# Kernel tuning notes

Measured on AMD Instinct MI355X. Metric: run time of the kernel, lower is better.

The kernel has to match this reference:

```python
import jax, jax.numpy as jnp
import numpy as np

B, S_T, P, D = 2, 8, 1369, 1024
S_STUDENT = 4
R = 128    # num_ref_samples
NS = 128   # num_shared_samples
K = 4      # topk
STUDENT_FRAMES = (0, 2, 4, 6)
EXTRA_FRAMES = (1, 3, 5, 7)   # teacher-only frames
HUBER_DELTA = 1.0
W1 = W2 = W3 = 1.0


def setup_inputs() -> dict:
    key = jax.random.key(0)
    k1, k2, k3, k4 = jax.random.split(key, 4)
    teacher_feats = jax.random.normal(k1, (B, S_T, P, D), dtype=jnp.float32)
    student_feats = jax.random.normal(k2, (B, S_STUDENT, P, D), dtype=jnp.float32)
    ref_perm = jax.random.permutation(k3, P)[:R].astype(jnp.int32)
    shared_perm = jax.random.permutation(k4, P)[:NS].astype(jnp.int32)
    return {"teacher_feats": teacher_feats, "student_feats": student_feats,
            "ref_perm": ref_perm, "shared_perm": shared_perm}


def _unit(x, eps):
    # F.normalize(x, dim=-1, eps=eps)
    n = jnp.linalg.norm(x, axis=-1, keepdims=True)
    return x / jnp.maximum(n, eps)


def _huber(pred, target):
    d = pred - target
    ad = jnp.abs(d)
    return jnp.where(ad < HUBER_DELTA, 0.5 * d * d, HUBER_DELTA * (ad - 0.5 * HUBER_DELTA))


def reference(teacher_feats, student_feats, ref_perm, shared_perm):
    t = jax.lax.stop_gradient(teacher_feats)  # teacher is always detached
    eps = 1e-8

    ref_t = t[:, STUDENT_FRAMES[0], ref_perm, :]        # [B,R,D]
    ref_s = student_feats[:, 0, ref_perm, :]            # [B,R,D]

    # top-K most similar teacher patches across extra frames
    extra_t = t[:, jnp.array(EXTRA_FRAMES)].reshape(B, len(EXTRA_FRAMES) * P, D)  # [B,M,D]
    sim = jnp.einsum('brd,bmd->brm', _unit(ref_t, 1e-12), _unit(extra_t, 1e-12))
    _, idx = jax.lax.top_k(sim, K)                      # [B,R,K]
    sim_high = jnp.take_along_axis(
        extra_t, idx.reshape(B, R * K)[:, :, None], axis=1).reshape(B, R, K, D)

    # vertex-ref / vertex-simhigh legs that don't depend on the shared frame
    b1_t = _unit(sim_high - ref_t[:, :, None, :], eps)  # [B,R,K,D]
    b1_s = _unit(sim_high - ref_s[:, :, None, :], eps)
    u2_t = _unit(ref_t[:, :, None, :] - sim_high, eps)  # [B,R,K,D]
    u2_s = _unit(ref_s[:, :, None, :] - sim_high, eps)

    s1 = jnp.float32(0.0)
    s2 = jnp.float32(0.0)
    s3 = jnp.float32(0.0)
    for f, t_idx in enumerate(STUDENT_FRAMES[1:]):
        sh_t = t[:, t_idx, shared_perm, :]              # [B,S,D]
        sh_s = student_feats[:, f + 1, shared_perm, :]  # [B,S,D]

        # angle1: vertex = ref; cos(shared-ref, simhigh-ref)
        a1_t = jnp.einsum('brsd,brkd->brsk', _unit(sh_t[:, None] - ref_t[:, :, None], eps), b1_t)
        a1_s = jnp.einsum('brsd,brkd->brsk', _unit(sh_s[:, None] - ref_s[:, :, None], eps), b1_s)
        s1 = s1 + _huber(a1_s, jax.lax.stop_gradient(a1_t)).sum()

        # angle2: vertex = sim_high; cos(ref-simhigh, shared-simhigh)
        v2_t = _unit(sh_t[:, None, :, None, :] - sim_high[:, :, None], eps)  # [B,R,S,K,D]
        v2_s = _unit(sh_s[:, None, :, None, :] - sim_high[:, :, None], eps)
        a2_t = jnp.einsum('brkd,brskd->brsk', u2_t, v2_t)
        a2_s = jnp.einsum('brkd,brskd->brsk', u2_s, v2_s)
        s2 = s2 + _huber(a2_s, jax.lax.stop_gradient(a2_t)).sum()

        # angle3: vertex = shared; cos(ref-shared, simhigh-shared)
        u3_t = _unit(ref_t[:, :, None] - sh_t[:, None], eps)                 # [B,R,S,D]
        u3_s = _unit(ref_s[:, :, None] - sh_s[:, None], eps)
        v3_t = _unit(sim_high[:, :, None] - sh_t[:, None, :, None, :], eps)  # [B,R,S,K,D]
        v3_s = _unit(sim_high[:, :, None] - sh_s[:, None, :, None, :], eps)
        a3_t = jnp.einsum('brsd,brskd->brsk', u3_t, v3_t)
        a3_s = jnp.einsum('brsd,brskd->brsk', u3_s, v3_s)
        s3 = s3 + _huber(a3_s, jax.lax.stop_gradient(a3_t)).sum()

    total = B * R * NS * K * len(STUDENT_FRAMES[1:])
    return W1 * s1 / total + W2 * s2 / total + W3 * s3 / total
```

## Files before the change

### kernel.cpp

```cpp
#include <hip/hip_runtime.h>
#include <float.h>

#define B_  2
#define ST_ 8
#define SS_ 4
#define P_  1369
#define D_  1024
#define R_  128
#define NS_ 128
#define K_  4
#define M_  5476

#define OFF_INVN  0u
#define OFF_REFT  11008u
#define OFF_REFS  (OFF_REFT + 262144u)
#define OFF_PRRT  (OFF_REFS + 262144u)
#define OFF_PRRS  (OFF_PRRT + 256u)
#define OFF_IDX   (OFF_PRRS + 256u)
#define OFF_PRST  (OFF_IDX + 1024u)
#define OFF_PRSS  (OFF_PRST + 1024u)
#define OFF_PSS   (OFF_PRSS + 1024u)
#define OFF_IB1T  (OFF_PSS + 1024u)
#define OFF_IB1S  (OFF_IB1T + 1024u)
#define OFF_NSH   (OFF_IB1S + 1024u)
#define OFF_C     (OFF_NSH + 1536u)
#define CP_       1401856u

__device__ __forceinline__ float dot4(const float4 a, const float4 b) {
  return a.x*b.x + a.y*b.y + a.z*b.z + a.w*b.w;
}

__global__ __launch_bounds__(256) void k_extra_norms(const float* __restrict__ teacher,
                                                     float* __restrict__ invn) {
  int row = blockIdx.x * 4 + (threadIdx.x >> 6);
  int lane = threadIdx.x & 63;
  if (row >= B_ * M_) return;
  int b = row / M_, m = row % M_;
  int j = m / P_, p = m % P_;
  const float* src = teacher + (((size_t)b * ST_ + 1 + 2 * j) * P_ + p) * D_;
  float s = 0.f;
  #pragma unroll
  for (int it = 0; it < 4; ++it) {
    float4 v = *(const float4*)(src + (it * 64 + lane) * 4);
    s += dot4(v, v);
  }
  for (int o = 32; o; o >>= 1) s += __shfl_down(s, o);
  if (lane == 0) invn[row] = 1.f / fmaxf(sqrtf(s), 1e-12f);
}

__global__ __launch_bounds__(256) void k_shnorm(const float* __restrict__ teacher,
                                                const float* __restrict__ student,
                                                const int* __restrict__ shared_perm,
                                                float* __restrict__ nsh) {
  int row = blockIdx.x * 4 + (threadIdx.x >> 6);
  int lane = threadIdx.x & 63;
  if (row >= 2 * B_ * 3 * NS_) return;
  int rid = row % (B_ * 3 * NS_);
  int is_stu = row / (B_ * 3 * NS_);
  int b = rid / (3 * NS_);
  int rem = rid % (3 * NS_);
  int f = rem / NS_, s = rem % NS_;
  int p = shared_perm[s];
  const float* src = is_stu
      ? student + (((size_t)b * SS_ + 1 + f) * P_ + p) * D_
      : teacher + (((size_t)b * ST_ + 2 + 2 * f) * P_ + p) * D_;
  float acc = 0.f;
  #pragma unroll
  for (int it = 0; it < 4; ++it) {
    float4 v = *(const float4*)(src + (it * 64 + lane) * 4);
    acc += dot4(v, v);
  }
  for (int o = 32; o; o >>= 1) acc += __shfl_down(acc, o);
  if (lane == 0) nsh[row] = acc;
}

__global__ __launch_bounds__(256) void k_ref_gather(const float* __restrict__ teacher,
                                                    const float* __restrict__ student,
                                                    const int* __restrict__ ref_perm,
                                                    float* __restrict__ reft,
                                                    float* __restrict__ refs,
                                                    float* __restrict__ prrt,
                                                    float* __restrict__ prrs) {
  int br = blockIdx.x;
  int b = br / R_, r = br % R_;
  int p = ref_perm[r];
  const float* st = teacher + (((size_t)b * ST_ + 0) * P_ + p) * D_;
  const float* ss = student + (((size_t)b * SS_ + 0) * P_ + p) * D_;
  float* dt = reft + (size_t)br * D_;
  float* dsp = refs + (size_t)br * D_;
  int t = threadIdx.x;
  float4 vt = *(const float4*)(st + t * 4);
  float4 vs = *(const float4*)(ss + t * 4);
  *(float4*)(dt + t * 4) = vt;
  *(float4*)(dsp + t * 4) = vs;
  float at = dot4(vt, vt);
  float as = dot4(vs, vs);
  for (int o = 32; o; o >>= 1) { at += __shfl_down(at, o); as += __shfl_down(as, o); }
  __shared__ float red[16];
  int w = t >> 6, lane = t & 63;
  if (lane == 0) { red[w] = at; red[8 + w] = as; }
  __syncthreads();
  if (t == 0) {
    prrt[br] = red[0] + red[1] + red[2] + red[3];
    prrs[br] = red[8] + red[9] + red[10] + red[11];
  }
}

__global__ __launch_bounds__(256) void k_sim_gemm(const float* __restrict__ teacher,
                                                  const float* __restrict__ reft,
                                                  float* __restrict__ Cp) {
  const int bid = blockIdx.x;
  const int kq  = bid & 3;
  const int rest = bid >> 2;
  const int b   = rest / 172;
  const int rem = rest % 172;
  const int rt  = rem / 86;
  const int mt  = rem % 86;
  const int r0 = rt * 64, m0 = mt * 64;
  __shared__ __align__(16) float Al[32 * 68];
  __shared__ __align__(16) float El[32 * 68];
  const int t = threadIdx.x;
  const int tx = t & 15, ty = t >> 4;
  const int lr = t >> 3;
  const int lk = (t & 7) * 4;
  const float* arow0 = reft + (size_t)(b * R_ + r0 + lr) * D_;
  const float* arow1 = reft + (size_t)(b * R_ + r0 + 32 + lr) * D_;
  const float* erow0; const float* erow1; bool ev0, ev1;
  {
    int m = m0 + lr; ev0 = m < M_;
    int mm = ev0 ? m : 0; int j = mm / P_, p = mm % P_;
    erow0 = teacher + (((size_t)b * ST_ + 1 + 2 * j) * P_ + p) * D_;
    m = m0 + 32 + lr; ev1 = m < M_;
    mm = ev1 ? m : 0; j = mm / P_; p = mm % P_;
    erow1 = teacher + (((size_t)b * ST_ + 1 + 2 * j) * P_ + p) * D_;
  }
  float acc[4][4];
  #pragma unroll
  for (int i = 0; i < 4; ++i)
    #pragma unroll
    for (int j = 0; j < 4; ++j) acc[i][j] = 0.f;

  const int kbeg = kq * 256, kend = kbeg + 256;
  for (int kc = kbeg; kc < kend; kc += 32) {
    __syncthreads();
    float4 a0 = *(const float4*)(arow0 + kc + lk);
    float4 a1 = *(const float4*)(arow1 + kc + lk);
    float4 e0 = ev0 ? *(const float4*)(erow0 + kc + lk) : make_float4(0, 0, 0, 0);
    float4 e1 = ev1 ? *(const float4*)(erow1 + kc + lk) : make_float4(0, 0, 0, 0);
    Al[(lk + 0) * 68 + lr] = a0.x; Al[(lk + 1) * 68 + lr] = a0.y;
    Al[(lk + 2) * 68 + lr] = a0.z; Al[(lk + 3) * 68 + lr] = a0.w;
    Al[(lk + 0) * 68 + 32 + lr] = a1.x; Al[(lk + 1) * 68 + 32 + lr] = a1.y;
    Al[(lk + 2) * 68 + 32 + lr] = a1.z; Al[(lk + 3) * 68 + 32 + lr] = a1.w;
    El[(lk + 0) * 68 + lr] = e0.x; El[(lk + 1) * 68 + lr] = e0.y;
    El[(lk + 2) * 68 + lr] = e0.z; El[(lk + 3) * 68 + lr] = e0.w;
    El[(lk + 0) * 68 + 32 + lr] = e1.x; El[(lk + 1) * 68 + 32 + lr] = e1.y;
    El[(lk + 2) * 68 + 32 + lr] = e1.z; El[(lk + 3) * 68 + 32 + lr] = e1.w;
    __syncthreads();
    #pragma unroll
    for (int kk = 0; kk < 32; ++kk) {
      float4 av = *(const float4*)&Al[kk * 68 + ty * 4];
      float4 ev = *(const float4*)&El[kk * 68 + tx * 4];
      acc[0][0] += av.x * ev.x; acc[0][1] += av.x * ev.y; acc[0][2] += av.x * ev.z; acc[0][3] += av.x * ev.w;
      acc[1][0] += av.y * ev.x; acc[1][1] += av.y * ev.y; acc[1][2] += av.y * ev.z; acc[1][3] += av.y * ev.w;
      acc[2][0] += av.z * ev.x; acc[2][1] += av.z * ev.y; acc[2][2] += av.z * ev.z; acc[2][3] += av.z * ev.w;
      acc[3][0] += av.w * ev.x; acc[3][1] += av.w * ev.y; acc[3][2] += av.w * ev.z; acc[3][3] += av.w * ev.w;
    }
  }
  const int mbase = m0 + tx * 4;
  float* cbase = Cp + (size_t)kq * CP_;
  #pragma unroll
  for (int i = 0; i < 4; ++i) {
    int r = r0 + ty * 4 + i;
    float* crow = cbase + (size_t)(b * R_ + r) * M_;
    if (mbase + 3 < M_) {
      *(float4*)(crow + mbase) = make_float4(acc[i][0], acc[i][1], acc[i][2], acc[i][3]);
    } else {
      if (mbase + 0 < M_) crow[mbase + 0] = acc[i][0];
      if (mbase + 1 < M_) crow[mbase + 1] = acc[i][1];
      if (mbase + 2 < M_) crow[mbase + 2] = acc[i][2];
      if (mbase + 3 < M_) crow[mbase + 3] = acc[i][3];
    }
  }
}

__device__ __forceinline__ void topk_insert(float v, int m, float bv[4], int bi[4]) {
  bool better3 = (v > bv[3]) || (v == bv[3] && m < bi[3]);
  if (!better3) return;
  int pos = 3;
  while (pos > 0) {
    bool better = (v > bv[pos - 1]) || (v == bv[pos - 1] && m < bi[pos - 1]);
    if (better) { bv[pos] = bv[pos - 1]; bi[pos] = bi[pos - 1]; --pos; }
    else break;
  }
  bv[pos] = v; bi[pos] = m;
}

__global__ __launch_bounds__(256) void k_topk(const float* __restrict__ Cp,
                                              const float* __restrict__ invn,
                                              int* __restrict__ idxout) {
  int br = blockIdx.x;
  int b = br / R_;
  const float* r0 = Cp + 0 * (size_t)CP_ + (size_t)br * M_;
  const float* r1 = Cp + 1 * (size_t)CP_ + (size_t)br * M_;
  const float* r2 = Cp + 2 * (size_t)CP_ + (size_t)br * M_;
  const float* r3 = Cp + 3 * (size_t)CP_ + (size_t)br * M_;
  const float* w = invn + (size_t)b * M_;
  int t = threadIdx.x;
  float bv[4] = {-FLT_MAX, -FLT_MAX, -FLT_MAX, -FLT_MAX};
  int   bi[4] = {0x7fffffff, 0x7fffffff, 0x7fffffff, 0x7fffffff};
  for (int m = t; m < M_; m += 256) {
    float v = ((r0[m] + r1[m]) + (r2[m] + r3[m])) * w[m];
    topk_insert(v, m, bv, bi);
  }

  #pragma unroll
  for (int o = 1; o < 64; o <<= 1) {
    float ov[4]; int oi[4];
    #pragma unroll
    for (int q = 0; q < 4; ++q) {
      ov[q] = __shfl_xor(bv[q], o);
      oi[q] = __shfl_xor(bi[q], o);
    }
    #pragma unroll
    for (int q = 0; q < 4; ++q) topk_insert(ov[q], oi[q], bv, bi);
  }

  __shared__ float sv[16];
  __shared__ int   si[16];
  int wv = t >> 6, lane = t & 63;
  if (lane == 0) {
    #pragma unroll
    for (int q = 0; q < 4; ++q) { sv[wv * 4 + q] = bv[q]; si[wv * 4 + q] = bi[q]; }
  }
  __syncthreads();
  if (t == 0) {
    float tv[4] = {-FLT_MAX, -FLT_MAX, -FLT_MAX, -FLT_MAX};
    int   ti[4] = {0x7fffffff, 0x7fffffff, 0x7fffffff, 0x7fffffff};
    #pragma unroll
    for (int e = 0; e < 16; ++e) topk_insert(sv[e], si[e], tv, ti);
    #pragma unroll
    for (int q = 0; q < 4; ++q) idxout[br * 4 + q] = ti[q];
  }
}

__global__ __launch_bounds__(256) void k_prep(const float* __restrict__ teacher,
                                              const float* __restrict__ reft,
                                              const float* __restrict__ refs,
                                              const int* __restrict__ idx,
                                              float* __restrict__ prst,
                                              float* __restrict__ prss,
                                              float* __restrict__ pss,
                                              float* __restrict__ ib1t,
                                              float* __restrict__ ib1s) {
  int br = blockIdx.x;
  int b = br / R_;
  int w = threadIdx.x >> 6, lane = threadIdx.x & 63;
  int m = idx[br * 4 + w];
  int j = m / P_, p = m % P_;
  const float* sim = teacher + (((size_t)b * ST_ + 1 + 2 * j) * P_ + p) * D_;
  const float* rt = reft + (size_t)br * D_;
  const float* rs = refs + (size_t)br * D_;
  float s_ss = 0, s_rt = 0, s_rs = 0, s_dt = 0, s_ds = 0;
  #pragma unroll
  for (int it = 0; it < 4; ++it) {
    int d = (it * 64 + lane) * 4;
    float4 svv = *(const float4*)(sim + d);
    float4 tvv = *(const float4*)(rt + d);
    float4 uvv = *(const float4*)(rs + d);
    s_ss += dot4(svv, svv);
    s_rt += dot4(svv, tvv);
    s_rs += dot4(svv, uvv);
    float4 dt = make_float4(svv.x - tvv.x, svv.y - tvv.y, svv.z - tvv.z, svv.w - tvv.w);
    float4 ds = make_float4(svv.x - uvv.x, svv.y - uvv.y, svv.z - uvv.z, svv.w - uvv.w);
    s_dt += dot4(dt, dt);
    s_ds += dot4(ds, ds);
  }
  for (int o = 32; o; o >>= 1) {
    s_ss += __shfl_down(s_ss, o); s_rt += __shfl_down(s_rt, o); s_rs += __shfl_down(s_rs, o);
    s_dt += __shfl_down(s_dt, o); s_ds += __shfl_down(s_ds, o);
  }
  if (lane == 0) {
    int o = br * 4 + w;
    pss[o] = s_ss; prst[o] = s_rt; prss[o] = s_rs;
    ib1t[o] = 1.f / fmaxf(sqrtf(s_dt), 1e-8f);
    ib1s[o] = 1.f / fmaxf(sqrtf(s_ds), 1e-8f);
  }
}

__device__ __forceinline__ float huber1(float d) {
  float ad = fabsf(d);
  return (ad < 1.0f) ? 0.5f * d * d : (ad - 0.5f);
}

__global__ __launch_bounds__(256) void k_loss(const float* __restrict__ teacher,
                                              const float* __restrict__ student,
                                              const int* __restrict__ shared_perm,
                                              const int* __restrict__ idx,
                                              const float* __restrict__ reft,
                                              const float* __restrict__ refs,
                                              const float* __restrict__ prrt,
                                              const float* __restrict__ prrs,
                                              const float* __restrict__ prst,
                                              const float* __restrict__ prss,
                                              const float* __restrict__ pss,
                                              const float* __restrict__ ib1t,
                                              const float* __restrict__ ib1s,
                                              const float* __restrict__ nsh,
                                              float* __restrict__ out) {
  int br = blockIdx.x, f = blockIdx.y, sc = blockIdx.z;
  int b = br / R_;
  int tf = 2 + 2 * f;
  int sf = 1 + f;
  __shared__ __align__(16) float Lsim[4][1024];
  __shared__ __align__(16) float Lrt[1024];
  __shared__ __align__(16) float Lrs[1024];
  __shared__ int sperm[128];
  __shared__ float Lns[2][64];
  __shared__ float scal[22];
  __shared__ float wred[4];
  int t = threadIdx.x;
  {
    const float* rt = reft + (size_t)br * D_;
    const float* rs = refs + (size_t)br * D_;
    *(float4*)&Lrt[t * 4] = *(const float4*)(rt + t * 4);
    *(float4*)&Lrs[t * 4] = *(const float4*)(rs + t * 4);
    #pragma unroll
    for (int k = 0; k < 4; ++k) {
      int m = idx[br * 4 + k]; int j = m / P_, p = m % P_;
      const float* sim = teacher + (((size_t)b * ST_ + 1 + 2 * j) * P_ + p) * D_;
      *(float4*)&Lsim[k][t * 4] = *(const float4*)(sim + t * 4);
    }
  }
  if (t < 128) sperm[t] = shared_perm[t];
  if (t < 64) {
    int o = (b * 3 + f) * NS_ + sc * 64 + t;
    Lns[0][t] = nsh[o];
    Lns[1][t] = nsh[B_ * 3 * NS_ + o];
  }
  if (t < 4) {
    int o = br * 4 + t;
    scal[t] = prst[o]; scal[4 + t] = prss[o]; scal[8 + t] = pss[o];
    scal[12 + t] = ib1t[o]; scal[16 + t] = ib1s[o];
  }
  if (t == 4) scal[20] = prrt[br];
  if (t == 5) scal[21] = prrs[br];
  __syncthreads();

  const int g = t >> 2, gl = t & 3;
  const int s = sc * 64 + g;
  const int p = sperm[s];
  const float* sht = teacher + (((size_t)b * ST_ + tf) * P_ + p) * D_;
  const float* shs = student + (((size_t)b * SS_ + sf) * P_ + p) * D_;

  float qt0 = 0, qt1 = 0, qt2 = 0, qt3 = 0, qtr = 0;
  float qs0 = 0, qs1 = 0, qs2 = 0, qs3 = 0, qsr = 0;
  #pragma unroll 2
  for (int i = 0; i < 64; ++i) {
    int off = i * 16 + gl * 4;
    float4 a  = *(const float4*)(sht + off);
    float4 c  = *(const float4*)(shs + off);
    float4 v0 = *(const float4*)&Lsim[0][off];
    float4 v1 = *(const float4*)&Lsim[1][off];
    float4 v2 = *(const float4*)&Lsim[2][off];
    float4 v3 = *(const float4*)&Lsim[3][off];
    float4 r1 = *(const float4*)&Lrt[off];
    float4 r2 = *(const float4*)&Lrs[off];
    qt0 += dot4(a, v0); qt1 += dot4(a, v1); qt2 += dot4(a, v2); qt3 += dot4(a, v3);
    qtr += dot4(a, r1);
    qs0 += dot4(c, v0); qs1 += dot4(c, v1); qs2 += dot4(c, v2); qs3 += dot4(c, v3);
    qsr += dot4(c, r2);
  }
  #pragma unroll
  for (int o = 1; o <= 2; o <<= 1) {
    qt0 += __shfl_xor(qt0, o); qt1 += __shfl_xor(qt1, o);
    qt2 += __shfl_xor(qt2, o); qt3 += __shfl_xor(qt3, o);
    qtr += __shfl_xor(qtr, o);
    qs0 += __shfl_xor(qs0, o); qs1 += __shfl_xor(qs1, o);
    qs2 += __shfl_xor(qs2, o); qs3 += __shfl_xor(qs3, o);
    qsr += __shfl_xor(qsr, o);
  }
  const int k = gl;
  float qsim  = (gl == 0) ? qt0 : (gl == 1) ? qt1 : (gl == 2) ? qt2 : qt3;
  float qsimS = (gl == 0) ? qs0 : (gl == 1) ? qs1 : (gl == 2) ? qs2 : qs3;
  float qref = qtr, qrefS = qsr;
  float qss = Lns[0][g], qssS = Lns[1][g];

  float Prs_t = scal[k], Prs_s = scal[4 + k], Pss_k = scal[8 + k];
  float ibt = scal[12 + k], ibs = scal[16 + k];
  float Prr_t = scal[20], Prr_s = scal[21];
  float n1sq = qss - 2.f * qref + Prr_t;
  float i1 = 1.f / fmaxf(sqrtf(fmaxf(n1sq, 0.f)), 1e-8f);
  float n2sq = qss - 2.f * qsim + Pss_k;
  float i2 = 1.f / fmaxf(sqrtf(fmaxf(n2sq, 0.f)), 1e-8f);
  float a1t = (qsim - qref - Prs_t + Prr_t) * ibt * i1;
  float a2t = -(qsim - Pss_k - qref + Prs_t) * ibt * i2;
  float a3t = (qss - qsim - qref + Prs_t) * i1 * i2;
  float n1sqS = qssS - 2.f * qrefS + Prr_s;
  float i1s = 1.f / fmaxf(sqrtf(fmaxf(n1sqS, 0.f)), 1e-8f);
  float n2sqS = qssS - 2.f * qsimS + Pss_k;
  float i2s = 1.f / fmaxf(sqrtf(fmaxf(n2sqS, 0.f)), 1e-8f);
  float a1s = (qsimS - qrefS - Prs_s + Prr_s) * ibs * i1s;
  float a2s = -(qsimS - Pss_k - qrefS + Prs_s) * ibs * i2s;
  float a3s = (qssS - qsimS - qrefS + Prs_s) * i1s * i2s;
  float lacc = huber1(a1s - a1t) + huber1(a2s - a2t) + huber1(a3s - a3t);

  int w = t >> 6, lane = t & 63;
  for (int o = 32; o; o >>= 1) lacc += __shfl_down(lacc, o);
  if (lane == 0) wred[w] = lacc;
  __syncthreads();
  if (t == 0) {
    float ssum = wred[0] + wred[1] + wred[2] + wred[3];
    atomicAdd(out, ssum * (1.0f / 393216.0f));
  }
}

extern "C" void kernel_launch(void* const* d_in, const int* in_sizes, int n_in,
                              void* d_out, int out_size, void* d_ws, size_t ws_size,
                              hipStream_t stream) {
  const float* teacher = (const float*)d_in[0];
  const float* student = (const float*)d_in[1];
  const int* ref_perm = (const int*)d_in[2];
  const int* shared_perm = (const int*)d_in[3];
  float* ws = (float*)d_ws;
  float* invn = ws + OFF_INVN;
  float* reft = ws + OFF_REFT;
  float* refs = ws + OFF_REFS;
  float* prrt = ws + OFF_PRRT;
  float* prrs = ws + OFF_PRRS;
  int*   idx  = (int*)(ws + OFF_IDX);
  float* prst = ws + OFF_PRST;
  float* prss = ws + OFF_PRSS;
  float* pss  = ws + OFF_PSS;
  float* ib1t = ws + OFF_IB1T;
  float* ib1s = ws + OFF_IB1S;
  float* nsh  = ws + OFF_NSH;
  float* Cp   = ws + OFF_C;

  hipMemsetAsync(d_out, 0, sizeof(float), stream);

  k_extra_norms<<<(B_ * M_ + 3) / 4, 256, 0, stream>>>(teacher, invn);
  k_shnorm<<<(2 * B_ * 3 * NS_ + 3) / 4, 256, 0, stream>>>(teacher, student,
                                                           shared_perm, nsh);
  k_ref_gather<<<B_ * R_, 256, 0, stream>>>(teacher, student, ref_perm,
                                            reft, refs, prrt, prrs);
  k_sim_gemm<<<1376, 256, 0, stream>>>(teacher, reft, Cp);
  k_topk<<<B_ * R_, 256, 0, stream>>>(Cp, invn, idx);
  k_prep<<<B_ * R_, 256, 0, stream>>>(teacher, reft, refs, idx,
                                      prst, prss, pss, ib1t, ib1s);
  k_loss<<<dim3(B_ * R_, 3, 2), 256, 0, stream>>>(teacher, student, shared_perm, idx,
                                                  reft, refs, prrt, prrs,
                                                  prst, prss, pss, ib1t, ib1s,
                                                  nsh, (float*)d_out);
}
```

Measured before the change: 320.5 us.

## Merge prep kernels, split top-k across blocks, widen loss kernel per block

After: 305.4 us. -4.7%, faster.

```diff
diff --git a/kernel.cpp b/kernel.cpp
--- a/kernel.cpp
+++ b/kernel.cpp
@@ -23,86 +23,90 @@
 #define OFF_IB1T  (OFF_PSS + 1024u)
 #define OFF_IB1S  (OFF_IB1T + 1024u)
 #define OFF_NSH   (OFF_IB1S + 1024u)
-#define OFF_C     (OFF_NSH + 1536u)
+#define OFF_CANDV (OFF_NSH + 1536u)
+#define OFF_CANDI (OFF_CANDV + 4096u)
+#define OFF_C     (OFF_CANDI + 4096u)
 #define CP_       1401856u
+
+#define NA_BLOCKS 2738
+#define NB_BLOCKS 384
+#define NC_BLOCKS 256
 
 __device__ __forceinline__ float dot4(const float4 a, const float4 b) {
   return a.x*b.x + a.y*b.y + a.z*b.z + a.w*b.w;
 }
 
-__global__ __launch_bounds__(256) void k_extra_norms(const float* __restrict__ teacher,
-                                                     float* __restrict__ invn) {
-  int row = blockIdx.x * 4 + (threadIdx.x >> 6);
-  int lane = threadIdx.x & 63;
-  if (row >= B_ * M_) return;
-  int b = row / M_, m = row % M_;
-  int j = m / P_, p = m % P_;
-  const float* src = teacher + (((size_t)b * ST_ + 1 + 2 * j) * P_ + p) * D_;
-  float s = 0.f;
-  #pragma unroll
-  for (int it = 0; it < 4; ++it) {
-    float4 v = *(const float4*)(src + (it * 64 + lane) * 4);
-    s += dot4(v, v);
-  }
-  for (int o = 32; o; o >>= 1) s += __shfl_down(s, o);
-  if (lane == 0) invn[row] = 1.f / fmaxf(sqrtf(s), 1e-12f);
-}
-
-__global__ __launch_bounds__(256) void k_shnorm(const float* __restrict__ teacher,
-                                                const float* __restrict__ student,
-                                                const int* __restrict__ shared_perm,
-                                                float* __restrict__ nsh) {
-  int row = blockIdx.x * 4 + (threadIdx.x >> 6);
-  int lane = threadIdx.x & 63;
-  if (row >= 2 * B_ * 3 * NS_) return;
-  int rid = row % (B_ * 3 * NS_);
-  int is_stu = row / (B_ * 3 * NS_);
-  int b = rid / (3 * NS_);
-  int rem = rid % (3 * NS_);
-  int f = rem / NS_, s = rem % NS_;
-  int p = shared_perm[s];
-  const float* src = is_stu
-      ? student + (((size_t)b * SS_ + 1 + f) * P_ + p) * D_
-      : teacher + (((size_t)b * ST_ + 2 + 2 * f) * P_ + p) * D_;
-  float acc = 0.f;
-  #pragma unroll
-  for (int it = 0; it < 4; ++it) {
-    float4 v = *(const float4*)(src + (it * 64 + lane) * 4);
-    acc += dot4(v, v);
-  }
-  for (int o = 32; o; o >>= 1) acc += __shfl_down(acc, o);
-  if (lane == 0) nsh[row] = acc;
-}
-
-__global__ __launch_bounds__(256) void k_ref_gather(const float* __restrict__ teacher,
-                                                    const float* __restrict__ student,
-                                                    const int* __restrict__ ref_perm,
-                                                    float* __restrict__ reft,
-                                                    float* __restrict__ refs,
-                                                    float* __restrict__ prrt,
-                                                    float* __restrict__ prrs) {
-  int br = blockIdx.x;
-  int b = br / R_, r = br % R_;
-  int p = ref_perm[r];
-  const float* st = teacher + (((size_t)b * ST_ + 0) * P_ + p) * D_;
-  const float* ss = student + (((size_t)b * SS_ + 0) * P_ + p) * D_;
-  float* dt = reft + (size_t)br * D_;
-  float* dsp = refs + (size_t)br * D_;
-  int t = threadIdx.x;
-  float4 vt = *(const float4*)(st + t * 4);
-  float4 vs = *(const float4*)(ss + t * 4);
-  *(float4*)(dt + t * 4) = vt;
-  *(float4*)(dsp + t * 4) = vs;
-  float at = dot4(vt, vt);
-  float as = dot4(vs, vs);
-  for (int o = 32; o; o >>= 1) { at += __shfl_down(at, o); as += __shfl_down(as, o); }
-  __shared__ float red[16];
-  int w = t >> 6, lane = t & 63;
-  if (lane == 0) { red[w] = at; red[8 + w] = as; }
-  __syncthreads();
-  if (t == 0) {
-    prrt[br] = red[0] + red[1] + red[2] + red[3];
-    prrs[br] = red[8] + red[9] + red[10] + red[11];
+__global__ __launch_bounds__(256) void k_prep0(const float* __restrict__ teacher,
+                                               const float* __restrict__ student,
+                                               const int* __restrict__ ref_perm,
+                                               const int* __restrict__ shared_perm,
+                                               float* __restrict__ invn,
+                                               float* __restrict__ nsh,
+                                               float* __restrict__ reft,
+                                               float* __restrict__ refs,
+                                               float* __restrict__ prrt,
+                                               float* __restrict__ prrs) {
+  const int bid = blockIdx.x;
+  const int t = threadIdx.x;
+  if (bid < NA_BLOCKS) {
+    int row = bid * 4 + (t >> 6);
+    int lane = t & 63;
+    if (row >= B_ * M_) return;
+    int b = row / M_, m = row % M_;
+    int j = m / P_, p = m % P_;
+    const float* src = teacher + (((size_t)b * ST_ + 1 + 2 * j) * P_ + p) * D_;
+    float s = 0.f;
+    #pragma unroll
+    for (int it = 0; it < 4; ++it) {
+      float4 v = *(const float4*)(src + (it * 64 + lane) * 4);
+      s += dot4(v, v);
+    }
+    for (int o = 32; o; o >>= 1) s += __shfl_down(s, o);
+    if (lane == 0) invn[row] = 1.f / fmaxf(sqrtf(s), 1e-12f);
+  } else if (bid < NA_BLOCKS + NB_BLOCKS) {
+    int row = (bid - NA_BLOCKS) * 4 + (t >> 6);
+    int lane = t & 63;
+    if (row >= 2 * B_ * 3 * NS_) return;
+    int rid = row % (B_ * 3 * NS_);
+    int is_stu = row / (B_ * 3 * NS_);
+    int b = rid / (3 * NS_);
+    int rem = rid % (3 * NS_);
+    int f = rem / NS_, s = rem % NS_;
+    int p = shared_perm[s];
+    const float* src = is_stu
+        ? student + (((size_t)b * SS_ + 1 + f) * P_ + p) * D_
+        : teacher + (((size_t)b * ST_ + 2 + 2 * f) * P_ + p) * D_;
+    float acc = 0.f;
+    #pragma unroll
+    for (int it = 0; it < 4; ++it) {
+      float4 v = *(const float4*)(src + (it * 64 + lane) * 4);
+      acc += dot4(v, v);
+    }
+    for (int o = 32; o; o >>= 1) acc += __shfl_down(acc, o);
+    if (lane == 0) nsh[row] = acc;
+  } else {
+    int br = bid - (NA_BLOCKS + NB_BLOCKS);
+    int b = br / R_, r = br % R_;
+    int p = ref_perm[r];
+    const float* st = teacher + (((size_t)b * ST_ + 0) * P_ + p) * D_;
+    const float* ss = student + (((size_t)b * SS_ + 0) * P_ + p) * D_;
+    float* dt = reft + (size_t)br * D_;
+    float* dsp = refs + (size_t)br * D_;
+    float4 vt = *(const float4*)(st + t * 4);
+    float4 vs = *(const float4*)(ss + t * 4);
+    *(float4*)(dt + t * 4) = vt;
+    *(float4*)(dsp + t * 4) = vs;
+    float at = dot4(vt, vt);
+    float as = dot4(vs, vs);
+    for (int o = 32; o; o >>= 1) { at += __shfl_down(at, o); as += __shfl_down(as, o); }
+    __shared__ float red[16];
+    int w = t >> 6, lane = t & 63;
+    if (lane == 0) { red[w] = at; red[8 + w] = as; }
+    __syncthreads();
+    if (t == 0) {
+      prrt[br] = red[0] + red[1] + red[2] + red[3];
+      prrs[br] = red[8] + red[9] + red[10] + red[11];
+    }
   }
 }
 
@@ -195,42 +199,43 @@
   bv[pos] = v; bi[pos] = m;
 }
 
-__global__ __launch_bounds__(256) void k_topk(const float* __restrict__ Cp,
-                                              const float* __restrict__ invn,
-                                              int* __restrict__ idxout) {
-  int br = blockIdx.x;
+__global__ __launch_bounds__(256) void k_topk1(const float* __restrict__ Cp,
+                                               const float* __restrict__ invn,
+                                               float* __restrict__ candv,
+                                               int* __restrict__ candi) {
+  int bid = blockIdx.x;
+  int br = bid >> 2, q = bid & 3;
   int b = br / R_;
   const float* r0 = Cp + 0 * (size_t)CP_ + (size_t)br * M_;
   const float* r1 = Cp + 1 * (size_t)CP_ + (size_t)br * M_;
   const float* r2 = Cp + 2 * (size_t)CP_ + (size_t)br * M_;
   const float* r3 = Cp + 3 * (size_t)CP_ + (size_t)br * M_;
   const float* w = invn + (size_t)b * M_;
+  const int mbeg = q * 1369, mend = mbeg + 1369;
   int t = threadIdx.x;
   float bv[4] = {-FLT_MAX, -FLT_MAX, -FLT_MAX, -FLT_MAX};
   int   bi[4] = {0x7fffffff, 0x7fffffff, 0x7fffffff, 0x7fffffff};
-  for (int m = t; m < M_; m += 256) {
+  for (int m = mbeg + t; m < mend; m += 256) {
     float v = ((r0[m] + r1[m]) + (r2[m] + r3[m])) * w[m];
     topk_insert(v, m, bv, bi);
   }
-
   #pragma unroll
   for (int o = 1; o < 64; o <<= 1) {
     float ov[4]; int oi[4];
     #pragma unroll
-    for (int q = 0; q < 4; ++q) {
-      ov[q] = __shfl_xor(bv[q], o);
-      oi[q] = __shfl_xor(bi[q], o);
-    }
-    #pragma unroll
-    for (int q = 0; q < 4; ++q) topk_insert(ov[q], oi[q], bv, bi);
-  }
-
+    for (int qq = 0; qq < 4; ++qq) {
+      ov[qq] = __shfl_xor(bv[qq], o);
+      oi[qq] = __shfl_xor(bi[qq], o);
+    }
+    #pragma unroll
+    for (int qq = 0; qq < 4; ++qq) topk_insert(ov[qq], oi[qq], bv, bi);
+  }
   __shared__ float sv[16];
   __shared__ int   si[16];
   int wv = t >> 6, lane = t & 63;
   if (lane == 0) {
     #pragma unroll
-    for (int q = 0; q < 4; ++q) { sv[wv * 4 + q] = bv[q]; si[wv * 4 + q] = bi[q]; }
+    for (int qq = 0; qq < 4; ++qq) { sv[wv * 4 + qq] = bv[qq]; si[wv * 4 + qq] = bi[qq]; }
   }
   __syncthreads();
   if (t == 0) {
@@ -239,14 +244,16 @@
     #pragma unroll
     for (int e = 0; e < 16; ++e) topk_insert(sv[e], si[e], tv, ti);
     #pragma unroll
-    for (int q = 0; q < 4; ++q) idxout[br * 4 + q] = ti[q];
+    for (int qq = 0; qq < 4; ++qq) { candv[bid * 4 + qq] = tv[qq]; candi[bid * 4 + qq] = ti[qq]; }
   }
 }
 
 __global__ __launch_bounds__(256) void k_prep(const float* __restrict__ teacher,
                                               const float* __restrict__ reft,
                                               const float* __restrict__ refs,
-                                              const int* __restrict__ idx,
+                                              const float* __restrict__ candv,
+                                              const int* __restrict__ candi,
+                                              int* __restrict__ idxout,
                                               float* __restrict__ prst,
                                               float* __restrict__ prss,
                                               float* __restrict__ pss,
@@ -254,8 +261,32 @@
                                               float* __restrict__ ib1s) {
   int br = blockIdx.x;
   int b = br / R_;
-  int w = threadIdx.x >> 6, lane = threadIdx.x & 63;
-  int m = idx[br * 4 + w];
+  int t = threadIdx.x;
+  __shared__ int sidx[4];
+  if (t < 64) {
+    float v = -FLT_MAX; int ix = 0x7fffffff;
+    if (t < 16) { v = candv[br * 16 + t]; ix = candi[br * 16 + t]; }
+    float bv[4] = {v, -FLT_MAX, -FLT_MAX, -FLT_MAX};
+    int   bi[4] = {ix, 0x7fffffff, 0x7fffffff, 0x7fffffff};
+    #pragma unroll
+    for (int o = 1; o <= 8; o <<= 1) {
+      float ov[4]; int oi[4];
+      #pragma unroll
+      for (int q = 0; q < 4; ++q) {
+        ov[q] = __shfl_xor(bv[q], o);
+        oi[q] = __shfl_xor(bi[q], o);
+      }
+      #pragma unroll
+      for (int q = 0; q < 4; ++q) topk_insert(ov[q], oi[q], bv, bi);
+    }
+    if (t == 0) {
+      #pragma unroll
+      for (int q = 0; q < 4; ++q) { sidx[q] = bi[q]; idxout[br * 4 + q] = bi[q]; }
+    }
+  }
+  __syncthreads();
+  int w = t >> 6, lane = t & 63;
+  int m = sidx[w];
   int j = m / P_, p = m % P_;
   const float* sim = teacher + (((size_t)b * ST_ + 1 + 2 * j) * P_ + p) * D_;
   const float* rt = reft + (size_t)br * D_;
@@ -307,7 +338,7 @@
                                               const float* __restrict__ ib1s,
                                               const float* __restrict__ nsh,
                                               float* __restrict__ out) {
-  int br = blockIdx.x, f = blockIdx.y, sc = blockIdx.z;
+  int br = blockIdx.x, f = blockIdx.y;
   int b = br / R_;
   int tf = 2 + 2 * f;
   int sf = 1 + f;
@@ -315,7 +346,7 @@
   __shared__ __align__(16) float Lrt[1024];
   __shared__ __align__(16) float Lrs[1024];
   __shared__ int sperm[128];
-  __shared__ float Lns[2][64];
+  __shared__ float Lns[2][128];
   __shared__ float scal[22];
   __shared__ float wred[4];
   int t = threadIdx.x;
@@ -331,9 +362,9 @@
       *(float4*)&Lsim[k][t * 4] = *(const float4*)(sim + t * 4);
     }
   }
-  if (t < 128) sperm[t] = shared_perm[t];
-  if (t < 64) {
-    int o = (b * 3 + f) * NS_ + sc * 64 + t;
+  if (t < 128) {
+    sperm[t] = shared_perm[t];
+    int o = (b * 3 + f) * NS_ + t;
     Lns[0][t] = nsh[o];
     Lns[1][t] = nsh[B_ * 3 * NS_ + o];
   }
@@ -347,62 +378,85 @@
   __syncthreads();
 
   const int g = t >> 2, gl = t & 3;
-  const int s = sc * 64 + g;
-  const int p = sperm[s];
-  const float* sht = teacher + (((size_t)b * ST_ + tf) * P_ + p) * D_;
-  const float* shs = student + (((size_t)b * SS_ + sf) * P_ + p) * D_;
-
-  float qt0 = 0, qt1 = 0, qt2 = 0, qt3 = 0, qtr = 0;
-  float qs0 = 0, qs1 = 0, qs2 = 0, qs3 = 0, qsr = 0;
+  const int s0 = g, s1 = g + 64;
+  const int p0 = sperm[s0], p1 = sperm[s1];
+  const float* sht0 = teacher + (((size_t)b * ST_ + tf) * P_ + p0) * D_;
+  const float* sht1 = teacher + (((size_t)b * ST_ + tf) * P_ + p1) * D_;
+  const float* shs0 = student + (((size_t)b * SS_ + sf) * P_ + p0) * D_;
+  const float* shs1 = student + (((size_t)b * SS_ + sf) * P_ + p1) * D_;
+
+  float qtA0 = 0, qtA1 = 0, qtA2 = 0, qtA3 = 0, qtrA = 0;
+  float qsA0 = 0, qsA1 = 0, qsA2 = 0, qsA3 = 0, qsrA = 0;
+  float qtB0 = 0, qtB1 = 0, qtB2 = 0, qtB3 = 0, qtrB = 0;
+  float qsB0 = 0, qsB1 = 0, qsB2 = 0, qsB3 = 0, qsrB = 0;
   #pragma unroll 2
   for (int i = 0; i < 64; ++i) {
     int off = i * 16 + gl * 4;
-    float4 a  = *(const float4*)(sht + off);
-    float4 c  = *(const float4*)(shs + off);
+    float4 a0 = *(const float4*)(sht0 + off);
+    float4 a1 = *(const float4*)(sht1 + off);
+    float4 c0 = *(const float4*)(shs0 + off);
+    float4 c1 = *(const float4*)(shs1 + off);
     float4 v0 = *(const float4*)&Lsim[0][off];
     float4 v1 = *(const float4*)&Lsim[1][off];
     float4 v2 = *(const float4*)&Lsim[2][off];
     float4 v3 = *(const float4*)&Lsim[3][off];
     float4 r1 = *(const float4*)&Lrt[off];
     float4 r2 = *(const float4*)&Lrs[off];
-    qt0 += dot4(a, v0); qt1 += dot4(a, v1); qt2 += dot4(a, v2); qt3 += dot4(a, v3);
-    qtr += dot4(a, r1);
-    qs0 += dot4(c, v0); qs1 += dot4(c, v1); qs2 += dot4(c, v2); qs3 += dot4(c, v3);
-    qsr += dot4(c, r2);
+    qtA0 += dot4(a0, v0); qtA1 += dot4(a0, v1); qtA2 += dot4(a0, v2); qtA3 += dot4(a0, v3);
+    qtrA += dot4(a0, r1);
+    qsA0 += dot4(c0, v0); qsA1 += dot4(c0, v1); qsA2 += dot4(c0, v2); qsA3 += dot4(c0, v3);
+    qsrA += dot4(c0, r2);
+    qtB0 += dot4(a1, v0); qtB1 += dot4(a1, v1); qtB2 += dot4(a1, v2); qtB3 += dot4(a1, v3);
+    qtrB += dot4(a1, r1);
+    qsB0 += dot4(c1, v0); qsB1 += dot4(c1, v1); qsB2 += dot4(c1, v2); qsB3 += dot4(c1, v3);
+    qsrB += dot4(c1, r2);
   }
   #pragma unroll
   for (int o = 1; o <= 2; o <<= 1) {
-    qt0 += __shfl_xor(qt0, o); qt1 += __shfl_xor(qt1, o);
-    qt2 += __shfl_xor(qt2, o); qt3 += __shfl_xor(qt3, o);
-    qtr += __shfl_xor(qtr, o);
-    qs0 += __shfl_xor(qs0, o); qs1 += __shfl_xor(qs1, o);
-    qs2 += __shfl_xor(qs2, o); qs3 += __shfl_xor(qs3, o);
-    qsr += __shfl_xor(qsr, o);
+    qtA0 += __shfl_xor(qtA0, o); qtA1 += __shfl_xor(qtA1, o);
+    qtA2 += __shfl_xor(qtA2, o); qtA3 += __shfl_xor(qtA3, o);
+    qtrA += __shfl_xor(qtrA, o);
+    qsA0 += __shfl_xor(qsA0, o); qsA1 += __shfl_xor(qsA1, o);
+    qsA2 += __shfl_xor(qsA2, o); qsA3 += __shfl_xor(qsA3, o);
+    qsrA += __shfl_xor(qsrA, o);
+    qtB0 += __shfl_xor(qtB0, o); qtB1 += __shfl_xor(qtB1, o);
+    qtB2 += __shfl_xor(qtB2, o); qtB3 += __shfl_xor(qtB3, o);
+    qtrB += __shfl_xor(qtrB, o);
+    qsB0 += __shfl_xor(qsB0, o); qsB1 += __shfl_xor(qsB1, o);
+    qsB2 += __shfl_xor(qsB2, o); qsB3 += __shfl_xor(qsB3, o);
+    qsrB += __shfl_xor(qsrB, o);
   }
   const int k = gl;
-  float qsim  = (gl == 0) ? qt0 : (gl == 1) ? qt1 : (gl == 2) ? qt2 : qt3;
-  float qsimS = (gl == 0) ? qs0 : (gl == 1) ? qs1 : (gl == 2) ? qs2 : qs3;
-  float qref = qtr, qrefS = qsr;
-  float qss = Lns[0][g], qssS = Lns[1][g];
-
-  float Prs_t = scal[k], Prs_s = scal[4 + k], Pss_k = scal[8 + k];
-  float ibt = scal[12 + k], ibs = scal[16 + k];
-  float Prr_t = scal[20], Prr_s = scal[21];
-  float n1sq = qss - 2.f * qref + Prr_t;
-  float i1 = 1.f / fmaxf(sqrtf(fmaxf(n1sq, 0.f)), 1e-8f);
-  float n2sq = qss - 2.f * qsim + Pss_k;
-  float i2 = 1.f / fmaxf(sqrtf(fmaxf(n2sq, 0.f)), 1e-8f);
-  float a1t = (qsim - qref - Prs_t + Prr_t) * ibt * i1;
-  float a2t = -(qsim - Pss_k - qref + Prs_t) * ibt * i2;
-  float a3t = (qss - qsim - qref + Prs_t) * i1 * i2;
-  float n1sqS = qssS - 2.f * qrefS + Prr_s;
-  float i1s = 1.f / fmaxf(sqrtf(fmaxf(n1sqS, 0.f)), 1e-8f);
-  float n2sqS = qssS - 2.f * qsimS + Pss_k;
-  float i2s = 1.f / fmaxf(sqrtf(fmaxf(n2sqS, 0.f)), 1e-8f);
-  float a1s = (qsimS - qrefS - Prs_s + Prr_s) * ibs * i1s;
-  float a2s = -(qsimS - Pss_k - qrefS + Prs_s) * ibs * i2s;
-  float a3s = (qssS - qsimS - qrefS + Prs_s) * i1s * i2s;
-  float lacc = huber1(a1s - a1t) + huber1(a2s - a2t) + huber1(a3s - a3t);
+  const float Prs_t = scal[k], Prs_s = scal[4 + k], Pss_k = scal[8 + k];
+  const float ibt = scal[12 + k], ibs = scal[16 + k];
+  const float Prr_t = scal[20], Prr_s = scal[21];
+
+  auto epi = [&](float qsim, float qsimS, float qref, float qrefS,
+                 float qss, float qssS) -> float {
+    float n1sq = qss - 2.f * qref + Prr_t;
+    float i1 = 1.f / fmaxf(sqrtf(fmaxf(n1sq, 0.f)), 1e-8f);
+    float n2sq = qss - 2.f * qsim + Pss_k;
+    float i2 = 1.f / fmaxf(sqrtf(fmaxf(n2sq, 0.f)), 1e-8f);
+    float a1t = (qsim - qref - Prs_t + Prr_t) * ibt * i1;
+    float a2t = -(qsim - Pss_k - qref + Prs_t) * ibt * i2;
+    float a3t = (qss - qsim - qref + Prs_t) * i1 * i2;
+    float n1sqS = qssS - 2.f * qrefS + Prr_s;
+    float i1s = 1.f / fmaxf(sqrtf(fmaxf(n1sqS, 0.f)), 1e-8f);
+    float n2sqS = qssS - 2.f * qsimS + Pss_k;
+    float i2s = 1.f / fmaxf(sqrtf(fmaxf(n2sqS, 0.f)), 1e-8f);
+    float a1s = (qsimS - qrefS - Prs_s + Prr_s) * ibs * i1s;
+    float a2s = -(qsimS - Pss_k - qrefS + Prs_s) * ibs * i2s;
+    float a3s = (qssS - qsimS - qrefS + Prs_s) * i1s * i2s;
+    return huber1(a1s - a1t) + huber1(a2s - a2t) + huber1(a3s - a3t);
+  };
+
+  float qsimA  = (gl == 0) ? qtA0 : (gl == 1) ? qtA1 : (gl == 2) ? qtA2 : qtA3;
+  float qsimSA = (gl == 0) ? qsA0 : (gl == 1) ? qsA1 : (gl == 2) ? qsA2 : qsA3;
+  float qsimB  = (gl == 0) ? qtB0 : (gl == 1) ? qtB1 : (gl == 2) ? qtB2 : qtB3;
+  float qsimSB = (gl == 0) ? qsB0 : (gl == 1) ? qsB1 : (gl == 2) ? qsB2 : qsB3;
+
+  float lacc = epi(qsimA, qsimSA, qtrA, qsrA, Lns[0][s0], Lns[1][s0])
+             + epi(qsimB, qsimSB, qtrB, qsrB, Lns[0][s1], Lns[1][s1]);
 
   int w = t >> 6, lane = t & 63;
   for (int o = 32; o; o >>= 1) lacc += __shfl_down(lacc, o);
@@ -434,21 +488,20 @@
   float* ib1t = ws + OFF_IB1T;
   float* ib1s = ws + OFF_IB1S;
   float* nsh  = ws + OFF_NSH;
+  float* candv = ws + OFF_CANDV;
+  int*   candi = (int*)(ws + OFF_CANDI);
   float* Cp   = ws + OFF_C;
 
   hipMemsetAsync(d_out, 0, sizeof(float), stream);
 
-  k_extra_norms<<<(B_ * M_ + 3) / 4, 256, 0, stream>>>(teacher, invn);
-  k_shnorm<<<(2 * B_ * 3 * NS_ + 3) / 4, 256, 0, stream>>>(teacher, student,
-                                                           shared_perm, nsh);
-  k_ref_gather<<<B_ * R_, 256, 0, stream>>>(teacher, student, ref_perm,
-                                            reft, refs, prrt, prrs);
+  k_prep0<<<NA_BLOCKS + NB_BLOCKS + NC_BLOCKS, 256, 0, stream>>>(
+      teacher, student, ref_perm, shared_perm, invn, nsh, reft, refs, prrt, prrs);
   k_sim_gemm<<<1376, 256, 0, stream>>>(teacher, reft, Cp);
-  k_topk<<<B_ * R_, 256, 0, stream>>>(Cp, invn, idx);
-  k_prep<<<B_ * R_, 256, 0, stream>>>(teacher, reft, refs, idx,
+  k_topk1<<<1024, 256, 0, stream>>>(Cp, invn, candv, candi);
+  k_prep<<<B_ * R_, 256, 0, stream>>>(teacher, reft, refs, candv, candi, idx,
                                       prst, prss, pss, ib1t, ib1s);
-  k_loss<<<dim3(B_ * R_, 3, 2), 256, 0, stream>>>(teacher, student, shared_perm, idx,
-                                                  reft, refs, prrt, prrs,
-                                                  prst, prss, pss, ib1t, ib1s,
-                                                  nsh, (float*)d_out);
-}
+  k_loss<<<dim3(B_ * R_, 3), 256, 0, stream>>>(teacher, student, shared_perm, idx,
+                                               reft, refs, prrt, prrs,
+                                               prst, prss, pss, ib1t, ib1s,
+                                               nsh, (float*)d_out);
+}
```
